# Performance work log

Hardware: AMD Instinct MI355X
Metric: run time of the kernel (lower is better)

The kernel has to match this reference:

```python
import jax, jax.numpy as jnp
import numpy as np

B, T, D = 2, 2048, 1024
E, K, FF = 8, 2, 4096


def setup_inputs() -> dict:
    key = jax.random.key(0)
    ks = jax.random.split(key, 4)
    scale = 0.02
    return {
        "x": jax.random.normal(ks[0], (B, T, D), jnp.float32),
        "gate_w": jax.random.normal(ks[1], (D, E), jnp.float32) * scale,
        "gate_b": jnp.zeros((E,), jnp.float32),
        "w1": jax.random.normal(ks[2], (E, D, FF), jnp.float32) * scale,
        "b1": jnp.zeros((E, FF), jnp.float32),
        "w2": jax.random.normal(ks[3], (E, FF, D), jnp.float32) * scale,
        "b2": jnp.zeros((E, D), jnp.float32),
    }


def reference(x, gate_w, gate_b, w1, b1, w2, b2):
    # x: (B,T,D). Original runs every expert densely over all tokens then masks;
    # since mask*x == x at selected positions and output is re-masked, the math
    # equals: output[t] = sum_k softmax(topk_vals)[k] * expert_{idx_k}(x)[t].
    n_experts = w1.shape[0]
    gate_logits = x @ gate_w + gate_b                      # (B,T,E)
    topk_vals, topk_idx = jax.lax.top_k(gate_logits, K)    # (B,T,K)
    topk_w = jax.nn.softmax(topk_vals, axis=-1)            # (B,T,K)
    onehot = jax.nn.one_hot(topk_idx, n_experts, dtype=x.dtype)  # (B,T,K,E)
    comb = jnp.sum(onehot * topk_w[..., None], axis=2)     # (B,T,E) combine weights

    # Dense per-expert FFN over all tokens (faithful to original redundant compute)
    h = jax.nn.gelu(jnp.einsum('btd,edf->ebtf', x, w1) + b1[:, None, None, :],
                    approximate=False)                      # (E,B,T,FF)
    y = jnp.einsum('ebtf,efd->ebtd', h, w2) + b2[:, None, None, :]  # (E,B,T,D)
    output = jnp.einsum('ebtd,bte->btd', y, comb)           # (B,T,D)

    expert_counts = jnp.sum(onehot, axis=(0, 1, 2)).astype(jnp.float32)  # (E,)
    return output, gate_logits, topk_idx, expert_counts
```

## Files before the change

### kernel.cpp

```cpp
#include <hip/hip_runtime.h>
#include <math.h>

#define NTOK 4096
#define DIM  1024
#define NE   8
#define FF   4096

#define OUT_LOGITS 4194304
#define OUT_IDX    4227072
#define OUT_CNT    4235264

typedef unsigned short u16;
typedef __bf16 bf16x8 __attribute__((ext_vector_type(8)));
typedef float  f32x4  __attribute__((ext_vector_type(4)));

__device__ __forceinline__ u16 f2bf(float f) {
  union { float f; unsigned u; } v; v.f = f;
  unsigned r = v.u + 0x7fffu + ((v.u >> 16) & 1u);
  return (u16)(r >> 16);
}

__device__ __forceinline__ float gelu_f(float v) {
  float u = v * (0.7978845608f + 0.0356774081f * v * v);
  float e = __expf(2.f * u);
  float t = 1.f - 2.f / (e + 1.f);
  return 0.5f * v * (1.f + t);
}

__device__ __forceinline__ void gload_lds16(const u16* g, u16* l) {
  __builtin_amdgcn_global_load_lds(
      (const __attribute__((address_space(1))) void*)(g),
      (__attribute__((address_space(3))) void*)(l), 16, 0, 0);
}

__global__ __launch_bounds__(256) void transpose_cvt_kernel(const float* __restrict__ in,
                                                            u16* __restrict__ out,
                                                            int R, int C) {
  __shared__ float tile[64][68];
  in  += (size_t)blockIdx.z * R * C;
  out += (size_t)blockIdx.z * R * C;
  int c0 = blockIdx.x * 64, r0 = blockIdx.y * 64;
  int t = threadIdx.x;
  int cr = (t & 15) * 4, rr = t >> 4;
  #pragma unroll
  for (int p = 0; p < 4; p++) {
    float4 v = *(const float4*)(in + (size_t)(r0 + rr + p * 16) * C + c0 + cr);
    *(float4*)&tile[rr + p * 16][cr] = v;
  }
  __syncthreads();
  int c = t >> 2, rb = (t & 3) * 4;
  u16* orow = out + (size_t)(c0 + c) * R + r0;
  #pragma unroll
  for (int it = 0; it < 4; it++) {
    int r = it * 16 + rb;
    ushort4 o;
    o.x = f2bf(tile[r + 0][c]);
    o.y = f2bf(tile[r + 1][c]);
    o.z = f2bf(tile[r + 2][c]);
    o.w = f2bf(tile[r + 3][c]);
    *(ushort4*)(orow + r) = o;
  }
}

__global__ __launch_bounds__(256) void gate_kernel(const float* __restrict__ x,
                                                   const float* __restrict__ gw,
                                                   const float* __restrict__ gb,
                                                   float* __restrict__ out,
                                                   int2* __restrict__ tk_idx,
                                                   float2* __restrict__ tk_w) {
  int wave = threadIdx.x >> 6, lane = threadIdx.x & 63;
  int token = blockIdx.x * 4 + wave;
  const float* xr = x + (size_t)token * DIM + lane * 16;
  float acc[NE];
  #pragma unroll
  for (int e = 0; e < NE; e++) acc[e] = 0.f;
  #pragma unroll
  for (int c = 0; c < 16; c += 4) {
    float4 xv = *(const float4*)(xr + c);
    const float* gwr = gw + (size_t)(lane * 16 + c) * NE;
    float xs[4] = {xv.x, xv.y, xv.z, xv.w};
    #pragma unroll
    for (int q = 0; q < 4; q++)
      #pragma unroll
      for (int e = 0; e < NE; e++)
        acc[e] += xs[q] * gwr[q * NE + e];
  }
  #pragma unroll
  for (int off = 32; off; off >>= 1)
    #pragma unroll
    for (int e = 0; e < NE; e++)
      acc[e] += __shfl_down(acc[e], off);

  if (lane == 0) {
    float lg[NE];
    #pragma unroll
    for (int e = 0; e < NE; e++) {
      lg[e] = acc[e] + gb[e];
      out[OUT_LOGITS + token * NE + e] = lg[e];
    }
    int i0 = 0; float v0 = lg[0];
    #pragma unroll
    for (int e = 1; e < NE; e++) if (lg[e] > v0) { v0 = lg[e]; i0 = e; }
    int i1 = -1; float v1 = -1e30f;
    #pragma unroll
    for (int e = 0; e < NE; e++) if (e != i0 && lg[e] > v1) { v1 = lg[e]; i1 = e; }
    float ex = expf(v1 - v0);
    float s = 1.f + ex;
    out[OUT_IDX + token * 2]     = (float)i0;
    out[OUT_IDX + token * 2 + 1] = (float)i1;
    tk_idx[token] = make_int2(i0, i1);
    tk_w[token]   = make_float2(1.f / s, ex / s);
  }
}

__global__ __launch_bounds__(512) void build_lists_kernel(
    const int2* __restrict__ tk_idx, const float2* __restrict__ tk_w,
    int* __restrict__ counts, int* __restrict__ offsets,
    int* __restrict__ tok_list, float* __restrict__ wt_list,
    float* __restrict__ cnt_out) {
  __shared__ int s_cnt[NE];
  int e = threadIdx.x >> 6, lane = threadIdx.x & 63;
  int cnt = 0;
  for (int base = 0; base < NTOK; base += 64) {
    int2 idx = tk_idx[base + lane];
    cnt += __popcll(__ballot(idx.x == e || idx.y == e));
  }
  if (lane == 0) s_cnt[e] = cnt;
  __syncthreads();
  int off = 0;
  for (int ee = 0; ee < e; ee++) off += s_cnt[ee];
  if (lane == 0) {
    counts[e]  = s_cnt[e];
    offsets[e] = off;
    cnt_out[e] = (float)s_cnt[e];
  }
  int pos = off;
  for (int base = 0; base < NTOK; base += 64) {
    int tok = base + lane;
    int2 idx = tk_idx[tok];
    float2 w = tk_w[tok];
    bool m0 = (idx.x == e), m1 = (idx.y == e);
    bool m = m0 || m1;
    unsigned long long mask = __ballot(m);
    if (m) {
      int p = pos + __popcll(mask & ((1ull << lane) - 1ull));
      tok_list[p] = tok;
      wt_list[p]  = m0 ? w.x : w.y;
    }
    pos += __popcll(mask);
  }
}

__global__ __launch_bounds__(256) void gather_x_kernel(const float* __restrict__ x,
                                                       const int* __restrict__ tok_list,
                                                       u16* __restrict__ xg) {
  int g = blockIdx.x;
  int tok = tok_list[g];
  int c = threadIdx.x * 4;
  float4 v = *(const float4*)(x + (size_t)tok * DIM + c);
  ushort4 o;
  o.x = f2bf(v.x); o.y = f2bf(v.y); o.z = f2bf(v.z); o.w = f2bf(v.w);
  *(ushort4*)(xg + (size_t)g * DIM + c) = o;
}

template <int MODE>
__global__ __launch_bounds__(256) void moe_gemm_kernel(
    const u16* __restrict__ Abase, const u16* __restrict__ Bbase,
    const float* __restrict__ bias,
    const int* __restrict__ counts, const int* __restrict__ offsets,
    const int* __restrict__ tok_list, const float* __restrict__ wt_list,
    u16* __restrict__ Hout, float* __restrict__ Out) {
  constexpr int KT = (MODE == 0) ? DIM : FF;
  constexpr int NT = (MODE == 0) ? FF : DIM;
  const int e  = blockIdx.z;
  const int ne = counts[e];
  const int m0 = blockIdx.y * 128;
  if (m0 >= ne) return;
  const int n0   = blockIdx.x * 128;
  const int offs = offsets[e];

  __shared__ u16 As[128 * 32];
  __shared__ u16 Bs[128 * 32];

  const int t = threadIdx.x;
  const int wave = t >> 6, lane = t & 63;
  const int quad = lane >> 4, l16 = lane & 15;
  const int wm = (wave & 1) * 64, wn = (wave >> 1) * 64;

  const int colA = (t & 3) * 8;
  const u16* aptr[2];
  const u16* bptr[2];
  #pragma unroll
  for (int p = 0; p < 2; p++) {
    int s  = m0 + p * 64 + (t >> 2);
    int sr = s < ne ? s : ne - 1;
    aptr[p] = Abase + (size_t)(offs + sr) * KT + colA;
    bptr[p] = Bbase + (size_t)e * NT * KT + (size_t)(n0 + p * 64 + (t >> 2)) * KT + colA;
  }
  u16* asDst[2] = { &As[t * 8], &As[2048 + t * 8] };
  u16* bsDst[2] = { &Bs[t * 8], &Bs[2048 + t * 8] };

  f32x4 acc[4][4];
  #pragma unroll
  for (int i = 0; i < 4; i++)
    #pragma unroll
    for (int j = 0; j < 4; j++)
      acc[i][j] = (f32x4){0.f, 0.f, 0.f, 0.f};

  for (int k0 = 0; k0 < KT; k0 += 32) {
    gload_lds16(aptr[0] + k0, asDst[0]);
    gload_lds16(aptr[1] + k0, asDst[1]);
    gload_lds16(bptr[0] + k0, bsDst[0]);
    gload_lds16(bptr[1] + k0, bsDst[1]);
    __syncthreads();
    bf16x8 af[4], bfr[4];
    #pragma unroll
    for (int i = 0; i < 4; i++) {
      af[i]  = *(const bf16x8*)&As[(wm + i * 16 + l16) * 32 + quad * 8];
      bfr[i] = *(const bf16x8*)&Bs[(wn + i * 16 + l16) * 32 + quad * 8];
    }
    #pragma unroll
    for (int i = 0; i < 4; i++)
      #pragma unroll
      for (int j = 0; j < 4; j++)
        acc[i][j] = __builtin_amdgcn_mfma_f32_16x16x32_bf16(af[i], bfr[j], acc[i][j], 0, 0, 0);
    __syncthreads();
  }

  if (MODE == 0) {
    const float* bb = bias + (size_t)e * FF + n0;
    #pragma unroll
    for (int i = 0; i < 4; i++) {
      #pragma unroll
      for (int r = 0; r < 4; r++) {
        int s = m0 + wm + i * 16 + quad * 4 + r;
        if (s < ne) {
          u16* hr = Hout + (size_t)(offs + s) * FF + n0;
          #pragma unroll
          for (int j = 0; j < 4; j++) {
            int nl = wn + j * 16 + l16;
            hr[nl] = f2bf(gelu_f(acc[i][j][r] + bb[nl]));
          }
        }
      }
    }
  } else {
    const float* bb = bias + (size_t)e * DIM + n0;
    #pragma unroll
    for (int i = 0; i < 4; i++) {
      #pragma unroll
      for (int r = 0; r < 4; r++) {
        int s = m0 + wm + i * 16 + quad * 4 + r;
        if (s < ne) {
          int   tok = tok_list[offs + s];
          float w   = wt_list[offs + s];
          float* orow = Out + (size_t)tok * DIM + n0;
          #pragma unroll
          for (int j = 0; j < 4; j++) {
            int nl = wn + j * 16 + l16;
            atomicAdd(&orow[nl], (acc[i][j][r] + bb[nl]) * w);
          }
        }
      }
    }
  }
}

extern "C" void kernel_launch(void* const* d_in, const int* in_sizes, int n_in,
                              void* d_out, int out_size, void* d_ws, size_t ws_size,
                              hipStream_t stream) {
  const float* x   = (const float*)d_in[0];
  const float* gw  = (const float*)d_in[1];
  const float* gb  = (const float*)d_in[2];
  const float* w1  = (const float*)d_in[3];
  const float* b1  = (const float*)d_in[4];
  const float* w2  = (const float*)d_in[5];
  const float* b2  = (const float*)d_in[6];
  float* out = (float*)d_out;
  char*  ws  = (char*)d_ws;

  u16* w1t = (u16*)(ws);
  u16* w2t = (u16*)(ws + 1ull * 67108864);
  u16* h   = (u16*)(ws + 2ull * 67108864);
  u16* xg  = (u16*)(ws + 3ull * 67108864);
  char* meta = ws + 3ull * 67108864 + 16777216;
  int*    counts   = (int*)(meta);
  int*    offsets  = (int*)(meta + 64);
  int*    tok_list = (int*)(meta + 128);
  float*  wt_list  = (float*)(meta + 128 + 32768);
  int2*   tk_idx   = (int2*)(meta + 128 + 2 * 32768);
  float2* tk_w     = (float2*)(meta + 128 + 2 * 32768 + 32768);
  (void)in_sizes; (void)n_in; (void)out_size; (void)ws_size;

  hipMemsetAsync(out, 0, (size_t)OUT_LOGITS * 4, stream);

  transpose_cvt_kernel<<<dim3(FF / 64, DIM / 64, NE), 256, 0, stream>>>(w1, w1t, DIM, FF);
  transpose_cvt_kernel<<<dim3(DIM / 64, FF / 64, NE), 256, 0, stream>>>(w2, w2t, FF, DIM);
  gate_kernel<<<NTOK / 4, 256, 0, stream>>>(x, gw, gb, out, tk_idx, tk_w);
  build_lists_kernel<<<1, 512, 0, stream>>>(tk_idx, tk_w, counts, offsets, tok_list, wt_list,
                                            out + OUT_CNT);
  gather_x_kernel<<<2 * NTOK, 256, 0, stream>>>(x, tok_list, xg);
  moe_gemm_kernel<0><<<dim3(FF / 128, NTOK / 128, NE), 256, 0, stream>>>(
      xg, w1t, b1, counts, offsets, tok_list, wt_list, h, nullptr);
  moe_gemm_kernel<1><<<dim3(DIM / 128, NTOK / 128, NE), 256, 0, stream>>>(
      h, w2t, b2, counts, offsets, tok_list, wt_list, nullptr, out);
}
```

Baseline: 661.6 us.

## Enlarge MoE GEMM tiles with double-buffered swizzled LDS staging

Replaces the 128x128, K=32 single-buffered expert GEMM with a templated 512-thread kernel. It uses larger tiles (256x256 for the first GEMM, 128x256 for the second), 64-wide K steps, and XOR-swizzled shared memory to avoid bank conflicts. The next K tile is loaded while the current one is computed, so each step needs only one barrier. Bias values are hoisted into registers. The large dynamic LDS allocation limits occupancy, and bigger M tiles waste more work on experts whose token counts do not fill a tile.

```diff
diff --git a/kernel.cpp b/kernel.cpp
--- a/kernel.cpp
+++ b/kernel.cpp
@@ -163,8 +163,8 @@
   *(ushort4*)(xg + (size_t)g * DIM + c) = o;
 }
 
-template <int MODE>
-__global__ __launch_bounds__(256) void moe_gemm_kernel(
+template <int MODE, int BM, int BN>
+__global__ __launch_bounds__(512, 2) void moe_gemm2_kernel(
     const u16* __restrict__ Abase, const u16* __restrict__ Bbase,
     const float* __restrict__ bias,
     const int* __restrict__ counts, const int* __restrict__ offsets,
@@ -172,94 +172,127 @@
     u16* __restrict__ Hout, float* __restrict__ Out) {
   constexpr int KT = (MODE == 0) ? DIM : FF;
   constexpr int NT = (MODE == 0) ? FF : DIM;
+  constexpr int LA = BM / 64;
+  constexpr int LB = BN / 64;
+  constexpr int MR = BM / 32;
+  constexpr int NR = BN / 64;
+  constexpr int ASZ = BM * 64;
+  constexpr int BSZ = BN * 64;
+  constexpr int NTILES = KT / 64;
+
+  extern __shared__ u16 sm[];
+
   const int e  = blockIdx.z;
   const int ne = counts[e];
-  const int m0 = blockIdx.y * 128;
+  const int m0 = blockIdx.y * BM;
   if (m0 >= ne) return;
-  const int n0   = blockIdx.x * 128;
+  const int n0   = blockIdx.x * BN;
   const int offs = offsets[e];
-
-  __shared__ u16 As[128 * 32];
-  __shared__ u16 Bs[128 * 32];
 
   const int t = threadIdx.x;
   const int wave = t >> 6, lane = t & 63;
   const int quad = lane >> 4, l16 = lane & 15;
-  const int wm = (wave & 1) * 64, wn = (wave >> 1) * 64;
-
-  const int colA = (t & 3) * 8;
-  const u16* aptr[2];
-  const u16* bptr[2];
-  #pragma unroll
-  for (int p = 0; p < 2; p++) {
-    int s  = m0 + p * 64 + (t >> 2);
-    int sr = s < ne ? s : ne - 1;
-    aptr[p] = Abase + (size_t)(offs + sr) * KT + colA;
-    bptr[p] = Bbase + (size_t)e * NT * KT + (size_t)(n0 + p * 64 + (t >> 2)) * KT + colA;
-  }
-  u16* asDst[2] = { &As[t * 8], &As[2048 + t * 8] };
-  u16* bsDst[2] = { &Bs[t * 8], &Bs[2048 + t * 8] };
-
-  f32x4 acc[4][4];
-  #pragma unroll
-  for (int i = 0; i < 4; i++)
-    #pragma unroll
-    for (int j = 0; j < 4; j++)
+  const int wmb = (wave & 1) * (BM / 2);
+  const int wnb = (wave >> 1) * (BN / 4);
+
+  const u16* aptr[LA];
+  const u16* bptr[LB];
+  #pragma unroll
+  for (int p = 0; p < LA; p++) {
+    int idx = p * 512 + t;
+    int row = idx >> 3, c = idx & 7;
+    int clog = c ^ (row & 7);
+    int s = m0 + row; if (s > ne - 1) s = ne - 1;
+    aptr[p] = Abase + (size_t)(offs + s) * KT + clog * 8;
+  }
+  #pragma unroll
+  for (int p = 0; p < LB; p++) {
+    int idx = p * 512 + t;
+    int row = idx >> 3, c = idx & 7;
+    int clog = c ^ (row & 7);
+    bptr[p] = Bbase + ((size_t)e * NT + n0 + row) * KT + clog * 8;
+  }
+
+  auto stage = [&](int buf, int k0) {
+    #pragma unroll
+    for (int p = 0; p < LA; p++)
+      gload_lds16(aptr[p] + k0, sm + buf * ASZ + (p * 512 + t) * 8);
+    #pragma unroll
+    for (int p = 0; p < LB; p++)
+      gload_lds16(bptr[p] + k0, sm + 2 * ASZ + buf * BSZ + (p * 512 + t) * 8);
+  };
+
+  const int xrow = l16 & 7;
+  const int xo[2] = { ((0 + quad) ^ xrow) * 8, ((4 + quad) ^ xrow) * 8 };
+  const int abase0 = (wmb + l16) * 64;
+  const int bbase0 = 2 * ASZ + (wnb + l16) * 64;
+
+  f32x4 acc[MR][NR];
+  #pragma unroll
+  for (int i = 0; i < MR; i++)
+    #pragma unroll
+    for (int j = 0; j < NR; j++)
       acc[i][j] = (f32x4){0.f, 0.f, 0.f, 0.f};
 
-  for (int k0 = 0; k0 < KT; k0 += 32) {
-    gload_lds16(aptr[0] + k0, asDst[0]);
-    gload_lds16(aptr[1] + k0, asDst[1]);
-    gload_lds16(bptr[0] + k0, bsDst[0]);
-    gload_lds16(bptr[1] + k0, bsDst[1]);
+  stage(0, 0);
+  __syncthreads();
+  int cur = 0;
+  for (int kt = 0; kt < NTILES; ++kt) {
+    if (kt + 1 < NTILES) stage(cur ^ 1, (kt + 1) * 64);
+    const u16* As = sm + cur * ASZ;
+    const u16* Bs = sm + cur * BSZ;
+    #pragma unroll
+    for (int kk = 0; kk < 2; kk++) {
+      bf16x8 a[MR], b[NR];
+      #pragma unroll
+      for (int i = 0; i < MR; i++) a[i] = *(const bf16x8*)&As[abase0 + i * 1024 + xo[kk]];
+      #pragma unroll
+      for (int j = 0; j < NR; j++) b[j] = *(const bf16x8*)&Bs[bbase0 + j * 1024 + xo[kk]];
+      #pragma unroll
+      for (int i = 0; i < MR; i++)
+        #pragma unroll
+        for (int j = 0; j < NR; j++)
+          acc[i][j] = __builtin_amdgcn_mfma_f32_16x16x32_bf16(a[i], b[j], acc[i][j], 0, 0, 0);
+    }
     __syncthreads();
-    bf16x8 af[4], bfr[4];
-    #pragma unroll
-    for (int i = 0; i < 4; i++) {
-      af[i]  = *(const bf16x8*)&As[(wm + i * 16 + l16) * 32 + quad * 8];
-      bfr[i] = *(const bf16x8*)&Bs[(wn + i * 16 + l16) * 32 + quad * 8];
-    }
-    #pragma unroll
-    for (int i = 0; i < 4; i++)
-      #pragma unroll
-      for (int j = 0; j < 4; j++)
-        acc[i][j] = __builtin_amdgcn_mfma_f32_16x16x32_bf16(af[i], bfr[j], acc[i][j], 0, 0, 0);
-    __syncthreads();
+    cur ^= 1;
   }
 
   if (MODE == 0) {
-    const float* bb = bias + (size_t)e * FF + n0;
-    #pragma unroll
-    for (int i = 0; i < 4; i++) {
+    const float* bb = bias + (size_t)e * FF + n0 + wnb;
+    float bc[NR];
+    #pragma unroll
+    for (int j = 0; j < NR; j++) bc[j] = bb[j * 16 + l16];
+    #pragma unroll
+    for (int i = 0; i < MR; i++) {
       #pragma unroll
       for (int r = 0; r < 4; r++) {
-        int s = m0 + wm + i * 16 + quad * 4 + r;
+        int s = m0 + wmb + i * 16 + quad * 4 + r;
         if (s < ne) {
-          u16* hr = Hout + (size_t)(offs + s) * FF + n0;
+          u16* hr = Hout + (size_t)(offs + s) * FF + n0 + wnb;
           #pragma unroll
-          for (int j = 0; j < 4; j++) {
-            int nl = wn + j * 16 + l16;
-            hr[nl] = f2bf(gelu_f(acc[i][j][r] + bb[nl]));
-          }
+          for (int j = 0; j < NR; j++)
+            hr[j * 16 + l16] = f2bf(gelu_f(acc[i][j][r] + bc[j]));
         }
       }
     }
   } else {
-    const float* bb = bias + (size_t)e * DIM + n0;
-    #pragma unroll
-    for (int i = 0; i < 4; i++) {
+    const float* bb = bias + (size_t)e * DIM + n0 + wnb;
+    float bc[NR];
+    #pragma unroll
+    for (int j = 0; j < NR; j++) bc[j] = bb[j * 16 + l16];
+    #pragma unroll
+    for (int i = 0; i < MR; i++) {
       #pragma unroll
       for (int r = 0; r < 4; r++) {
-        int s = m0 + wm + i * 16 + quad * 4 + r;
+        int s = m0 + wmb + i * 16 + quad * 4 + r;
         if (s < ne) {
           int   tok = tok_list[offs + s];
           float w   = wt_list[offs + s];
-          float* orow = Out + (size_t)tok * DIM + n0;
+          float* orow = Out + (size_t)tok * DIM + n0 + wnb;
           #pragma unroll
-          for (int j = 0; j < 4; j++) {
-            int nl = wn + j * 16 + l16;
-            atomicAdd(&orow[nl], (acc[i][j][r] + bb[nl]) * w);
-          }
+          for (int j = 0; j < NR; j++)
+            atomicAdd(&orow[j * 16 + l16], (acc[i][j][r] + bc[j]) * w);
         }
       }
     }
@@ -292,6 +325,15 @@
   float2* tk_w     = (float2*)(meta + 128 + 2 * 32768 + 32768);
   (void)in_sizes; (void)n_in; (void)out_size; (void)ws_size;
 
+  static bool attr_set = false;
+  if (!attr_set) {
+    hipFuncSetAttribute(reinterpret_cast<const void*>(moe_gemm2_kernel<0, 256, 256>),
+                        hipFuncAttributeMaxDynamicSharedMemorySize, 131072);
+    hipFuncSetAttribute(reinterpret_cast<const void*>(moe_gemm2_kernel<1, 128, 256>),
+                        hipFuncAttributeMaxDynamicSharedMemorySize, 98304);
+    attr_set = true;
+  }
+
   hipMemsetAsync(out, 0, (size_t)OUT_LOGITS * 4, stream);
 
   transpose_cvt_kernel<<<dim3(FF / 64, DIM / 64, NE), 256, 0, stream>>>(w1, w1t, DIM, FF);
@@ -300,8 +342,9 @@
   build_lists_kernel<<<1, 512, 0, stream>>>(tk_idx, tk_w, counts, offsets, tok_list, wt_list,
                                             out + OUT_CNT);
   gather_x_kernel<<<2 * NTOK, 256, 0, stream>>>(x, tok_list, xg);
-  moe_gemm_kernel<0><<<dim3(FF / 128, NTOK / 128, NE), 256, 0, stream>>>(
+
+  moe_gemm2_kernel<0, 256, 256><<<dim3(FF / 256, NTOK / 256, NE), 512, 131072, stream>>>(
       xg, w1t, b1, counts, offsets, tok_list, wt_list, h, nullptr);
-  moe_gemm_kernel<1><<<dim3(DIM / 128, NTOK / 128, NE), 256, 0, stream>>>(
+  moe_gemm2_kernel<1, 128, 256><<<dim3(DIM / 256, NTOK / 128, NE), 512, 98304, stream>>>(
       h, w2t, b2, counts, offsets, tok_list, wt_list, nullptr, out);
 }
```

New measurement: 620.8 us. -6.2%, faster.
